# Performance work log

Measured on AMD Instinct MI355X. Metric: run time of the kernel, lower is better.

## Reference

```python
import jax, jax.numpy as jnp
import numpy as np

B, N, PL = 8, 961, 50          # batch, sequence_len=(64-4)//2+1 squared, patch_len=3*4^2+2
HID = 200                       # int(4.0 * patch_len)
D, H, HD = 768, 12, 64          # embed_dim, num_heads, head_dim
MP = 1536                       # int(2.0 * embed_dim)


def setup_inputs() -> dict:
    key = jax.random.key(0)
    ks = jax.random.split(key, 16)
    w = lambda k, i, o: jax.random.normal(k, (i, o), jnp.float32) / np.float32(np.sqrt(i))
    b = lambda k, o: jax.random.normal(k, (o,), jnp.float32) * np.float32(0.01)
    return {
        "x": jax.random.normal(ks[0], (B, N, PL), jnp.float32),
        "W1": w(ks[1], PL, HID),   "b1": b(ks[2], HID),
        "W2": w(ks[3], HID, HID),  "b2": b(ks[4], HID),
        "W3": w(ks[5], HID, HID),  "b3": b(ks[6], HID),
        "W4": w(ks[7], HID, D),    "b4": b(ks[8], D),
        "Wruv": w(ks[9], D, 3 * D), "bruv": b(ks[10], 3 * D),
        "Wp1": w(ks[11], N * HD, MP), "bp1": b(ks[12], MP),
        "Wp2": w(ks[13], MP, 1),      "bp2": b(ks[14], 1),
    }


def reference(x, W1, b1, W2, b2, W3, b3, W4, b4, Wruv, bruv, Wp1, bp1, Wp2, bp2):
    Bs, Ns, _ = x.shape
    # pointwise MLP (note: original has NO activations, just stacked Linears)
    h = x.reshape(Bs * Ns, -1)
    h = (((h @ W1 + b1) @ W2 + b2) @ W3 + b3) @ W4 + b4           # (B*N, D)
    # fused r,u,v projection -> (3, H, B, N, HD)
    ruv = (h @ Wruv + bruv).reshape(Bs, Ns, 3, H, HD).transpose(2, 3, 0, 1, 4)
    r, u, v = ruv[0], ruv[1], ruv[2]                               # each (H, B, N, HD)
    attn = jax.nn.softmax(jnp.einsum('hbnd,hbmd->hbnm', r, u), axis=-1)
    o = jnp.einsum('hbnm,hbmd->hbnd', attn, v).reshape(H, Bs, Ns * HD)
    # per-head projection: weights are SHARED across heads (list built via [m]*H)
    q = (jnp.einsum('hbm,mp->hbp', o, Wp1) + bp1) @ Wp2 + bp2      # (H, B, 1)
    return q[..., 0].T                                             # (B, 12)
```

## Files before the change

kernel.cpp:

```cpp
#include <hip/hip_runtime.h>
#include <hip/hip_bf16.h>

#define TPB 256

typedef __attribute__((ext_vector_type(8))) short bf16x8;
typedef __attribute__((ext_vector_type(4))) float f32x4;

static __device__ __forceinline__ unsigned short f2bf(float f) {
  union { float f; unsigned int u; } x; x.f = f;
  unsigned int r = x.u + 0x7FFF + ((x.u >> 16) & 1);
  return (unsigned short)(r >> 16);
}
static __device__ __forceinline__ float bf2f(unsigned short h) {
  union { unsigned int u; float f; } x; x.u = ((unsigned int)h) << 16;
  return x.f;
}

#define MFMA16(a, b, c) __builtin_amdgcn_mfma_f32_16x16x32_bf16(a, b, c, 0, 0, 0)

__global__ __launch_bounds__(TPB) void fold_wp_fused_k(
    const float* __restrict__ A, const float* __restrict__ lastrow,
    const float* __restrict__ W, const float* __restrict__ bias,
    float* __restrict__ C, int K, int Nc, int gemmBlocks,
    const float* __restrict__ Wp1, const float* __restrict__ Wp2,
    float* __restrict__ wfold, int wpStart, int wpCount,
    const float* __restrict__ bp1, const float* __restrict__ bp2,
    float* __restrict__ out)
{
  __shared__ float As[64][68];
  __shared__ float Ws[64][68];
  __shared__ float red[4];
  int bid = blockIdx.x, tid = threadIdx.x;

  if (bid >= gemmBlocks) {
    int u = bid - gemmBlocks;
    int wv = tid >> 6, lane = tid & 63;
    if (u >= wpCount) {
      float s = 0.f;
      for (int i = tid; i < 1536; i += TPB) s += bp1[i] * Wp2[i];
#pragma unroll
      for (int off = 32; off >= 1; off >>= 1) s += __shfl_xor(s, off, 64);
      if (lane == 0) red[wv] = s;
      __syncthreads();
      if (tid < 96) out[tid] = red[0] + red[1] + red[2] + red[3] + bp2[0];
      return;
    }
    float* w2 = &As[0][0];
    for (int i = tid; i < 1536; i += TPB) w2[i] = Wp2[i];
    __syncthreads();
    int m = (wpStart + u) * 4 + wv;
    const float* row = Wp1 + (size_t)m * 1536;
    float s = 0.f;
#pragma unroll
    for (int k = 0; k < 6; ++k) {
      float4 a  = *(const float4*)(row + k * 256 + lane * 4);
      float4 ww = *(const float4*)&w2[k * 256 + lane * 4];
      s += a.x * ww.x + a.y * ww.y + a.z * ww.z + a.w * ww.w;
    }
#pragma unroll
    for (int off = 32; off >= 1; off >>= 1) s += __shfl_xor(s, off, 64);
    if (lane == 0) wfold[m] = s;
    return;
  }

  int col0 = bid * 64;
  int ty = tid >> 4, tx = tid & 15;
  float acc[4][4] = {};
  for (int k0 = 0; k0 < K; k0 += 64) {
#pragma unroll
    for (int i = 0; i < 16; ++i) {
      int idx = tid + i * TPB;
      int r = idx >> 6, kk = idx & 63;
      int gk = k0 + kk;
      float v = 0.f;
      if (gk < K) {
        if (r < 50) v = A[(size_t)r * K + gk];
        else if (r == 50) v = lastrow[gk];
      }
      As[kk][r] = v;
    }
#pragma unroll
    for (int i = 0; i < 16; ++i) {
      int idx = tid + i * TPB;
      int kk = idx >> 6, cc = idx & 63;
      int gk = k0 + kk, gc = col0 + cc;
      float v = 0.f;
      if (gk < K && gc < Nc) v = W[(size_t)gk * Nc + gc];
      Ws[kk][cc] = v;
    }
    __syncthreads();
#pragma unroll 8
    for (int kk = 0; kk < 64; ++kk) {
      float4 a4 = *(const float4*)&As[kk][ty * 4];
      float4 b4 = *(const float4*)&Ws[kk][tx * 4];
      float av[4] = {a4.x, a4.y, a4.z, a4.w};
      float bv[4] = {b4.x, b4.y, b4.z, b4.w};
#pragma unroll
      for (int i = 0; i < 4; ++i)
#pragma unroll
        for (int j = 0; j < 4; ++j)
          acc[i][j] = fmaf(av[i], bv[j], acc[i][j]);
    }
    __syncthreads();
  }
#pragma unroll
  for (int i = 0; i < 4; ++i) {
    int gr = ty * 4 + i;
    if (gr >= 51) continue;
#pragma unroll
    for (int j = 0; j < 4; ++j) {
      int gc = col0 + tx * 4 + j;
      if (gc >= Nc) continue;
      float v = acc[i][j];
      if (gr == 50) v += bias[gc];
      C[(size_t)gr * Nc + gc] = v;
    }
  }
}

__global__ __launch_bounds__(TPB) void fold4_fused_k(
    const float* __restrict__ aug3,
    const float* __restrict__ Wruv,
    const float* __restrict__ bruv,
    unsigned short* __restrict__ WfTh, unsigned short* __restrict__ WfTl,
    float* __restrict__ bfv,
    const float* __restrict__ x,
    unsigned short* __restrict__ xh, unsigned short* __restrict__ xl,
    unsigned short* __restrict__ xT,
    const float* __restrict__ Wp1, const float* __restrict__ Wp2,
    float* __restrict__ wfold, int wpStart, int wpCount)
{
  __shared__ float As[64][68];
  __shared__ float Ws[64][68];
  int bid = blockIdx.x, tid = threadIdx.x;

  if (bid >= 157) {
    int u = bid - 157;
    if (u >= wpCount) return;
    int wv = tid >> 6, lane = tid & 63;
    float* w2 = &As[0][0];
    for (int i = tid; i < 1536; i += TPB) w2[i] = Wp2[i];
    __syncthreads();
    int m = (wpStart + u) * 4 + wv;
    const float* row = Wp1 + (size_t)m * 1536;
    float s = 0.f;
#pragma unroll
    for (int k = 0; k < 6; ++k) {
      float4 a  = *(const float4*)(row + k * 256 + lane * 4);
      float4 ww = *(const float4*)&w2[k * 256 + lane * 4];
      s += a.x * ww.x + a.y * ww.y + a.z * ww.z + a.w * ww.w;
    }
#pragma unroll
    for (int off = 32; off >= 1; off >>= 1) s += __shfl_xor(s, off, 64);
    if (lane == 0) wfold[m] = s;
    return;
  }

  if (bid >= 36) {
    int row0 = (bid - 36) * 64;
#pragma unroll
    for (int i = 0; i < 16; ++i) {
      int idx = tid + i * TPB;
      int row = row0 + (idx >> 6), cc = idx & 63;
      if (row >= 7688) continue;
      float v = 0.f;
      if (cc < 50) v = x[(size_t)row * 50 + cc];
      else if (cc == 50) v = 1.0f;
      unsigned short hi = f2bf(v);
      xh[(size_t)row * 64 + cc] = hi;
      xl[(size_t)row * 64 + cc] = f2bf(v - bf2f(hi));
      int bb = row / 961;
      int nl = row - bb * 961;
      xT[((size_t)bb * 64 + cc) * 968 + nl] = hi;
    }
    return;
  }

  const int K = 768, Nc = 2304;
  const float* lastrow = aug3 + (size_t)50 * 768;
  int col0 = bid * 64;
  int ty = tid >> 4, tx = tid & 15;
  float acc[4][4] = {};
  for (int k0 = 0; k0 < K; k0 += 64) {
#pragma unroll
    for (int i = 0; i < 16; ++i) {
      int idx = tid + i * TPB;
      int r = idx >> 6, kk = idx & 63;
      int gk = k0 + kk;
      float v = 0.f;
      if (r < 50) v = aug3[(size_t)r * K + gk];
      else if (r == 50) v = lastrow[gk];
      As[kk][r] = v;
    }
#pragma unroll
    for (int i = 0; i < 16; ++i) {
      int idx = tid + i * TPB;
      int kk = idx >> 6, cc = idx & 63;
      Ws[kk][cc] = Wruv[(size_t)(k0 + kk) * Nc + col0 + cc];
    }
    __syncthreads();
#pragma unroll 8
    for (int kk = 0; kk < 64; ++kk) {
      float4 a4 = *(const float4*)&As[kk][ty * 4];
      float4 b4 = *(const float4*)&Ws[kk][tx * 4];
      float av[4] = {a4.x, a4.y, a4.z, a4.w};
      float bv[4] = {b4.x, b4.y, b4.z, b4.w};
#pragma unroll
      for (int i = 0; i < 4; ++i)
#pragma unroll
        for (int j = 0; j < 4; ++j)
          acc[i][j] = fmaf(av[i], bv[j], acc[i][j]);
    }
    __syncthreads();
  }
#pragma unroll
  for (int i = 0; i < 4; ++i) {
    int gr = ty * 4 + i;
    if (gr >= 51) continue;
#pragma unroll
    for (int j = 0; j < 4; ++j) {
      int gc = col0 + tx * 4 + j;
      float v = acc[i][j];
      if (gr == 50) {
        bfv[gc] = v + bruv[gc];
      } else {
        unsigned short hi = f2bf(v);
        size_t el = (size_t)gc * 64 + gr;
        WfTh[el] = hi;
        WfTl[el] = f2bf(v - bf2f(hi));
      }
    }
  }
}

__global__ __launch_bounds__(TPB) void prep_k(
    const unsigned short* __restrict__ WfTh,
    const unsigned short* __restrict__ WfTl,
    const float* __restrict__ bfv,
    const float* __restrict__ wfold,
    unsigned short* __restrict__ Mth,
    unsigned short* __restrict__ Mtl,
    float* __restrict__ wvf)
{
  __shared__ float Al[64][64];
  __shared__ float Bl[64][64];
  int bid = blockIdx.x, tid = threadIdx.x;

  if (bid < 12) {
    int h = bid;
    for (int idx = tid; idx < 4096; idx += TPB) {
      int d = idx >> 6, i = idx & 63;
      int colr = h * 64 + d, colu = 768 + h * 64 + d;
      float wr = 0.f, wu = 0.f;
      if (i < 50) {
        wr = bf2f(WfTh[(size_t)colr * 64 + i]) + bf2f(WfTl[(size_t)colr * 64 + i]);
        wu = bf2f(WfTh[(size_t)colu * 64 + i]) + bf2f(WfTl[(size_t)colu * 64 + i]);
      } else if (i == 50) {
        wr = bfv[colr];
        wu = bfv[colu];
      }
      Al[d][i] = wr;
      Bl[d][i] = wu;
    }
    __syncthreads();
    for (int idx = tid; idx < 4096; idx += TPB) {
      int j = idx >> 6, i = idx & 63;
      float m = 0.f;
#pragma unroll 8
      for (int d = 0; d < 64; ++d) m += Al[d][i] * Bl[d][j];
      unsigned short hi = f2bf(m);
      size_t el = ((size_t)h * 64 + j) * 64 + i;
      Mth[el] = hi;
      Mtl[el] = f2bf(m - bf2f(hi));
    }
    return;
  }

  int u = bid - 12;
  int h = u >> 4, nb = u & 15;
  for (int idx = tid; idx < 4096; idx += TPB) {
    int d = idx >> 6, f = idx & 63;
    int colv = 1536 + h * 64 + d;
    float wv = 0.f;
    if (f < 50)
      wv = bf2f(WfTh[(size_t)colv * 64 + f]) + bf2f(WfTl[(size_t)colv * 64 + f]);
    else if (f == 50)
      wv = bfv[colv];
    Al[d][f] = wv;
    int nl = idx >> 6, dd = idx & 63;
    int n = nb * 64 + nl;
    Bl[nl][dd] = (n <= 960) ? wfold[(size_t)n * 64 + dd] : 0.f;
  }
  __syncthreads();
  for (int idx = tid; idx < 4096; idx += TPB) {
    int nl = idx >> 6, f = idx & 63;
    int n = nb * 64 + nl;
    if (n > 960) continue;
    float s = 0.f;
#pragma unroll 8
    for (int d = 0; d < 64; ++d) s += Bl[nl][d] * Al[d][f];
    wvf[((size_t)h * 961 + n) * 64 + f] = s;
  }
}

__global__ __launch_bounds__(512) void attn_x_k(
    const unsigned short* __restrict__ xh,
    const unsigned short* __restrict__ xl,
    const unsigned short* __restrict__ xT,
    const unsigned short* __restrict__ Mth,
    const unsigned short* __restrict__ Mtl,
    const float* __restrict__ wvf,
    float* __restrict__ out)
{
  __shared__ unsigned short sh[24576];
  int bid = blockIdx.x;
  int tid = threadIdx.x;

  int qb = bid & 7, hb = bid >> 3;
  int h = hb >> 3, b = hb & 7;
  int n0 = qb * 128;
  int w = tid >> 6, lane = tid & 63;
  int g = lane >> 4, c = lane & 15;
  int xb = b * 961;
  unsigned short* Kbuf[2] = {sh, sh + 4096};
  unsigned short* Vbuf[2] = {sh + 8192, sh + 12288};
  unsigned short* pw = sh + 16384 + w * 1024;

  int srow = tid >> 3, ss = tid & 7;
  int sel = srow * 64 + 8 * (ss ^ (srow & 7));
  const unsigned short* ksrc = xh + (size_t)xb * 64 + ss * 8;
  const unsigned short* vsrc = xT + ((size_t)b * 64 + srow) * 968 + ss * 8;
  int4 kv0 = *(const int4*)(ksrc + (size_t)srow * 64);
  int4 vv0 = *(const int4*)(vsrc);

  int qrow = n0 + w * 16 + c;
  if (qrow > 960) qrow = 960;
  size_t rowb = (size_t)(xb + qrow) * 64;
  bf16x8 axh0 = *(const bf16x8*)&xh[rowb + g * 8];
  bf16x8 axh1 = *(const bf16x8*)&xh[rowb + 32 + g * 8];
  bf16x8 axl0 = *(const bf16x8*)&xl[rowb + g * 8];
  bf16x8 axl1 = *(const bf16x8*)&xl[rowb + 32 + g * 8];

  f32x4 zero4 = {0.f, 0.f, 0.f, 0.f};
  f32x4 zacc[4] = {zero4, zero4, zero4, zero4};
#pragma unroll
  for (int ct = 0; ct < 4; ++ct) {
    int j = c * 4 + ct;
    size_t mb = ((size_t)h * 64 + j) * 64;
    bf16x8 bh0 = *(const bf16x8*)&Mth[mb + g * 8];
    bf16x8 bh1 = *(const bf16x8*)&Mth[mb + 32 + g * 8];
    bf16x8 bl0 = *(const bf16x8*)&Mtl[mb + g * 8];
    bf16x8 bl1 = *(const bf16x8*)&Mtl[mb + 32 + g * 8];
    zacc[ct] = MFMA16(axh0, bh0, zacc[ct]);
    zacc[ct] = MFMA16(axh1, bh1, zacc[ct]);
    zacc[ct] = MFMA16(axl0, bh0, zacc[ct]);
    zacc[ct] = MFMA16(axl1, bh1, zacc[ct]);
    zacc[ct] = MFMA16(axh0, bl0, zacc[ct]);
    zacc[ct] = MFMA16(axh1, bl1, zacc[ct]);
  }
#pragma unroll
  for (int r = 0; r < 4; ++r) {
    unsigned short pb[4];
#pragma unroll
    for (int ct = 0; ct < 4; ++ct) pb[ct] = f2bf(zacc[ct][r]);
    int q = g * 4 + r;
    int e0 = (c * 4) ^ ((q & 7) * 8);
    *(unsigned int*)&pw[q * 64 + e0] =
        (unsigned int)pb[0] | ((unsigned int)pb[1] << 16);
    *(unsigned int*)&pw[q * 64 + e0 + 2] =
        (unsigned int)pb[2] | ((unsigned int)pb[3] << 16);
  }
  bf16x8 zf0 = *(const bf16x8*)&pw[c * 64 + ((g * 8) ^ ((c & 7) * 8))];
  bf16x8 zf1 = *(const bf16x8*)&pw[c * 64 + ((32 + g * 8) ^ ((c & 7) * 8))];

  bf16x8 ones;
#pragma unroll
  for (int i = 0; i < 8; ++i) ones[i] = (short)0x3F80;

  *(int4*)&Kbuf[0][sel] = kv0;
  *(int4*)&Vbuf[0][sel] = vv0;
  __syncthreads();

  f32x4 pxacc[4] = {zero4, zero4, zero4, zero4};
  f32x4 rowacc = zero4;

  unsigned short* Kc = Kbuf[0];
  unsigned short* Vc = Vbuf[0];
  unsigned short* Kn = Kbuf[1];
  unsigned short* Vn = Vbuf[1];

  for (int kt = 0; kt < 16; ++kt) {
    int4 pk, pv;
    bool pre = (kt < 15);
    if (pre) {
      int keyg = (kt + 1) * 64 + srow;
      int kcl = keyg > 960 ? 960 : keyg;
      pk = *(const int4*)(ksrc + (size_t)kcl * 64);
      pv = *(const int4*)(vsrc + (kt + 1) * 64);
    }

    f32x4 sa[4] = {zero4, zero4, zero4, zero4};
    __builtin_amdgcn_s_setprio(1);
#pragma unroll
    for (int ct = 0; ct < 4; ++ct) {
      int key = c * 4 + ct;
      int sw = (key & 7) * 8;
      bf16x8 k0 = *(const bf16x8*)&Kc[key * 64 + ((g * 8) ^ sw)];
      bf16x8 k1 = *(const bf16x8*)&Kc[key * 64 + ((32 + g * 8) ^ sw)];
      sa[ct] = MFMA16(zf0, k0, sa[ct]);
      sa[ct] = MFMA16(zf1, k1, sa[ct]);
    }
    __builtin_amdgcn_s_setprio(0);

    if (kt < 15) {
#pragma unroll
      for (int r = 0; r < 4; ++r) {
        unsigned short pb[4];
#pragma unroll
        for (int ct = 0; ct < 4; ++ct)
          pb[ct] = f2bf(__expf(sa[ct][r]));
        int q = g * 4 + r;
        int e0 = (c * 4) ^ ((q & 7) * 8);
        *(unsigned int*)&pw[q * 64 + e0] =
            (unsigned int)pb[0] | ((unsigned int)pb[1] << 16);
        *(unsigned int*)&pw[q * 64 + e0 + 2] =
            (unsigned int)pb[2] | ((unsigned int)pb[3] << 16);
      }
    } else {
#pragma unroll
      for (int r = 0; r < 4; ++r) {
        unsigned short pb[4];
#pragma unroll
        for (int ct = 0; ct < 4; ++ct) {
          int keyg = kt * 64 + c * 4 + ct;
          pb[ct] = (keyg <= 960) ? f2bf(__expf(sa[ct][r])) : (unsigned short)0;
        }
        int q = g * 4 + r;
        int e0 = (c * 4) ^ ((q & 7) * 8);
        *(unsigned int*)&pw[q * 64 + e0] =
            (unsigned int)pb[0] | ((unsigned int)pb[1] << 16);
        *(unsigned int*)&pw[q * 64 + e0 + 2] =
            (unsigned int)pb[2] | ((unsigned int)pb[3] << 16);
      }
    }

    if (pre) {
      *(int4*)&Kn[sel] = pk;
      *(int4*)&Vn[sel] = pv;
    }

    __builtin_amdgcn_s_setprio(1);
#pragma unroll
    for (int kk = 0; kk < 2; ++kk) {
      bf16x8 pa = *(const bf16x8*)&pw[c * 64 + ((kk * 32 + g * 8) ^ ((c & 7) * 8))];
      rowacc = MFMA16(pa, ones, rowacc);
#pragma unroll
      for (int dt = 0; dt < 4; ++dt) {
        int d = dt * 16 + c;
        bf16x8 vf = *(const bf16x8*)&Vc[d * 64 + ((kk * 32 + g * 8) ^ ((d & 7) * 8))];
        pxacc[dt] = MFMA16(pa, vf, pxacc[dt]);
      }
    }
    __builtin_amdgcn_s_setprio(0);

    __syncthreads();
    unsigned short* t;
    t = Kc; Kc = Kn; Kn = t;
    t = Vc; Vc = Vn; Vn = t;
  }

  int nbase = n0 + w * 16 + g * 4;
  float part = 0.f;
#pragma unroll
  for (int r = 0; r < 4; ++r) {
    int n = nbase + r;
    if (n > 960) continue;
    float inv = 1.f / rowacc[r];
    const float* wv = wvf + ((size_t)h * 961 + n) * 64;
#pragma unroll
    for (int dt = 0; dt < 4; ++dt)
      part += pxacc[dt][r] * inv * wv[dt * 16 + c];
  }
#pragma unroll
  for (int off = 32; off >= 1; off >>= 1) part += __shfl_xor(part, off, 64);
  float* red = (float*)sh;
  if (lane == 0) red[w] = part;
  __syncthreads();
  if (tid == 0) {
    float tot = red[0] + red[1] + red[2] + red[3] +
                red[4] + red[5] + red[6] + red[7];
    atomicAdd(&out[b * 12 + h], tot);
  }
}

extern "C" void kernel_launch(void* const* d_in, const int* in_sizes, int n_in,
                              void* d_out, int out_size, void* d_ws, size_t ws_size,
                              hipStream_t stream)
{
  const float* x    = (const float*)d_in[0];
  const float* W1   = (const float*)d_in[1];
  const float* b1   = (const float*)d_in[2];
  const float* W2   = (const float*)d_in[3];
  const float* b2   = (const float*)d_in[4];
  const float* W3   = (const float*)d_in[5];
  const float* b3   = (const float*)d_in[6];
  const float* W4   = (const float*)d_in[7];
  const float* b4   = (const float*)d_in[8];
  const float* Wruv = (const float*)d_in[9];
  const float* bruv = (const float*)d_in[10];
  const float* Wp1  = (const float*)d_in[11];
  const float* bp1  = (const float*)d_in[12];
  const float* Wp2  = (const float*)d_in[13];
  const float* bp2  = (const float*)d_in[14];
  float* out = (float*)d_out;

  char* base = (char*)d_ws;
  size_t off = 0;
  auto alloc = [&](size_t bytes) -> void* {
    void* p = base + off;
    off = (off + bytes + 255) & ~(size_t)255;
    return p;
  };
  float* aug1  = (float*)alloc(51 * 200 * 4);
  float* aug2  = (float*)alloc(51 * 200 * 4);
  float* aug3  = (float*)alloc(51 * 768 * 4);
  unsigned short* WfTh = (unsigned short*)alloc((size_t)2304 * 64 * 2);
  unsigned short* WfTl = (unsigned short*)alloc((size_t)2304 * 64 * 2);
  unsigned short* xh   = (unsigned short*)alloc((size_t)(7688 + 64) * 64 * 2);
  unsigned short* xl   = (unsigned short*)alloc((size_t)(7688 + 64) * 64 * 2);
  unsigned short* xT   = (unsigned short*)alloc((size_t)8 * 64 * 968 * 2 + 1024);
  unsigned short* Mth  = (unsigned short*)alloc((size_t)12 * 64 * 64 * 2);
  unsigned short* Mtl  = (unsigned short*)alloc((size_t)12 * 64 * 64 * 2);
  float* wvf   = (float*)alloc((size_t)12 * 961 * 64 * 4);
  float* bfv   = (float*)alloc(2304 * 4);
  float* wfold = (float*)alloc(61504 * 4);
  if (off > ws_size) return;

  dim3 tb(TPB);

  fold_wp_fused_k<<<dim3(4 + 3844 + 1), tb, 0, stream>>>(
      W1, b1, W2, b2, aug1, 200, 200, 4,
      Wp1, Wp2, wfold, 0, 3844, bp1, bp2, out);
  fold_wp_fused_k<<<dim3(4 + 3844), tb, 0, stream>>>(
      aug1, aug1 + 50 * 200, W3, b3, aug2, 200, 200, 4,
      Wp1, Wp2, wfold, 3844, 3844, bp1, bp2, out);
  fold_wp_fused_k<<<dim3(12 + 3844), tb, 0, stream>>>(
      aug2, aug2 + 50 * 200, W4, b4, aug3, 200, 768, 12,
      Wp1, Wp2, wfold, 7688, 3844, bp1, bp2, out);

  fold4_fused_k<<<dim3(157 + 3844), tb, 0, stream>>>(
      aug3, Wruv, bruv, WfTh, WfTl, bfv, x, xh, xl, xT,
      Wp1, Wp2, wfold, 11532, 3844);

  prep_k<<<dim3(204), tb, 0, stream>>>(WfTh, WfTl, bfv, wfold, Mth, Mtl, wvf);

  attn_x_k<<<dim3(768), dim3(512), 0, stream>>>(xh, xl, xT, Mth, Mtl, wvf, out);
}
```

Baseline: 317.6 us.

## Overlap Wp1 folding with attention and defer value projection to final kernel

Shrinks the Wp1·Wp2 folding spread across the earlier fold kernels and moves the remaining rows into extra blocks of the attention kernel, so that weight-streaming work overlaps with attention compute. The attention epilogue now writes the normalized P·V outputs to a large Y buffer instead of dotting them with a precomputed per-head wvf. A new final kernel contracts Y with wfold and the V projection weights to produce the outputs. The precomputed wvf stage is dropped, at the cost of an extra round trip of about 24MB through global memory and one more launch.

```diff
diff --git a/kernel.cpp b/kernel.cpp
--- a/kernel.cpp
+++ b/kernel.cpp
@@ -233,88 +233,78 @@
   }
 }
 
-__global__ __launch_bounds__(TPB) void prep_k(
+__global__ __launch_bounds__(TPB) void prepM_k(
     const unsigned short* __restrict__ WfTh,
     const unsigned short* __restrict__ WfTl,
     const float* __restrict__ bfv,
-    const float* __restrict__ wfold,
     unsigned short* __restrict__ Mth,
-    unsigned short* __restrict__ Mtl,
-    float* __restrict__ wvf)
+    unsigned short* __restrict__ Mtl)
 {
   __shared__ float Al[64][64];
   __shared__ float Bl[64][64];
-  int bid = blockIdx.x, tid = threadIdx.x;
-
-  if (bid < 12) {
-    int h = bid;
-    for (int idx = tid; idx < 4096; idx += TPB) {
-      int d = idx >> 6, i = idx & 63;
-      int colr = h * 64 + d, colu = 768 + h * 64 + d;
-      float wr = 0.f, wu = 0.f;
-      if (i < 50) {
-        wr = bf2f(WfTh[(size_t)colr * 64 + i]) + bf2f(WfTl[(size_t)colr * 64 + i]);
-        wu = bf2f(WfTh[(size_t)colu * 64 + i]) + bf2f(WfTl[(size_t)colu * 64 + i]);
-      } else if (i == 50) {
-        wr = bfv[colr];
-        wu = bfv[colu];
-      }
-      Al[d][i] = wr;
-      Bl[d][i] = wu;
-    }
-    __syncthreads();
-    for (int idx = tid; idx < 4096; idx += TPB) {
-      int j = idx >> 6, i = idx & 63;
-      float m = 0.f;
-#pragma unroll 8
-      for (int d = 0; d < 64; ++d) m += Al[d][i] * Bl[d][j];
-      unsigned short hi = f2bf(m);
-      size_t el = ((size_t)h * 64 + j) * 64 + i;
-      Mth[el] = hi;
-      Mtl[el] = f2bf(m - bf2f(hi));
-    }
-    return;
-  }
-
-  int u = bid - 12;
-  int h = u >> 4, nb = u & 15;
+  int h = blockIdx.x, tid = threadIdx.x;
+
   for (int idx = tid; idx < 4096; idx += TPB) {
-    int d = idx >> 6, f = idx & 63;
-    int colv = 1536 + h * 64 + d;
-    float wv = 0.f;
-    if (f < 50)
-      wv = bf2f(WfTh[(size_t)colv * 64 + f]) + bf2f(WfTl[(size_t)colv * 64 + f]);
-    else if (f == 50)
-      wv = bfv[colv];
-    Al[d][f] = wv;
-    int nl = idx >> 6, dd = idx & 63;
-    int n = nb * 64 + nl;
-    Bl[nl][dd] = (n <= 960) ? wfold[(size_t)n * 64 + dd] : 0.f;
+    int d = idx >> 6, i = idx & 63;
+    int colr = h * 64 + d, colu = 768 + h * 64 + d;
+    float wr = 0.f, wu = 0.f;
+    if (i < 50) {
+      wr = bf2f(WfTh[(size_t)colr * 64 + i]) + bf2f(WfTl[(size_t)colr * 64 + i]);
+      wu = bf2f(WfTh[(size_t)colu * 64 + i]) + bf2f(WfTl[(size_t)colu * 64 + i]);
+    } else if (i == 50) {
+      wr = bfv[colr];
+      wu = bfv[colu];
+    }
+    Al[d][i] = wr;
+    Bl[d][i] = wu;
   }
   __syncthreads();
   for (int idx = tid; idx < 4096; idx += TPB) {
-    int nl = idx >> 6, f = idx & 63;
-    int n = nb * 64 + nl;
-    if (n > 960) continue;
-    float s = 0.f;
+    int j = idx >> 6, i = idx & 63;
+    float m = 0.f;
 #pragma unroll 8
-    for (int d = 0; d < 64; ++d) s += Bl[nl][d] * Al[d][f];
-    wvf[((size_t)h * 961 + n) * 64 + f] = s;
-  }
-}
-
-__global__ __launch_bounds__(512) void attn_x_k(
+    for (int d = 0; d < 64; ++d) m += Al[d][i] * Bl[d][j];
+    unsigned short hi = f2bf(m);
+    size_t el = ((size_t)h * 64 + j) * 64 + i;
+    Mth[el] = hi;
+    Mtl[el] = f2bf(m - bf2f(hi));
+  }
+}
+
+__global__ __launch_bounds__(512) void attn_wp_y_k(
     const unsigned short* __restrict__ xh,
     const unsigned short* __restrict__ xl,
     const unsigned short* __restrict__ xT,
     const unsigned short* __restrict__ Mth,
     const unsigned short* __restrict__ Mtl,
-    const float* __restrict__ wvf,
-    float* __restrict__ out)
+    float* __restrict__ Y,
+    const float* __restrict__ Wp1, const float* __restrict__ Wp2,
+    float* __restrict__ wfold)
 {
   __shared__ unsigned short sh[24576];
   int bid = blockIdx.x;
   int tid = threadIdx.x;
+
+  if (bid >= 768) {
+    int u = bid - 768;
+    int wv = tid >> 6, lane = tid & 63;
+    float* w2 = (float*)sh;
+    for (int i = tid; i < 1536; i += 512) w2[i] = Wp2[i];
+    __syncthreads();
+    int m = 25600 + u * 8 + wv;
+    const float* row = Wp1 + (size_t)m * 1536;
+    float s = 0.f;
+#pragma unroll
+    for (int k = 0; k < 6; ++k) {
+      float4 a  = *(const float4*)(row + k * 256 + lane * 4);
+      float4 ww = *(const float4*)&w2[k * 256 + lane * 4];
+      s += a.x * ww.x + a.y * ww.y + a.z * ww.z + a.w * ww.w;
+    }
+#pragma unroll
+    for (int off = 32; off >= 1; off >>= 1) s += __shfl_xor(s, off, 64);
+    if (lane == 0) wfold[m] = s;
+    return;
+  }
 
   int qb = bid & 7, hb = bid >> 3;
   int h = hb >> 3, b = hb & 7;
@@ -470,27 +460,85 @@
   }
 
   int nbase = n0 + w * 16 + g * 4;
-  float part = 0.f;
+  float* yb = Y + (size_t)hb * 961 * 64;
 #pragma unroll
   for (int r = 0; r < 4; ++r) {
     int n = nbase + r;
     if (n > 960) continue;
     float inv = 1.f / rowacc[r];
-    const float* wv = wvf + ((size_t)h * 961 + n) * 64;
 #pragma unroll
     for (int dt = 0; dt < 4; ++dt)
-      part += pxacc[dt][r] * inv * wv[dt * 16 + c];
-  }
-#pragma unroll
-  for (int off = 32; off >= 1; off >>= 1) part += __shfl_xor(part, off, 64);
-  float* red = (float*)sh;
-  if (lane == 0) red[w] = part;
+      yb[(size_t)n * 64 + dt * 16 + c] = pxacc[dt][r] * inv;
+  }
+}
+
+__global__ __launch_bounds__(TPB) void final_k(
+    const float* __restrict__ Y,
+    const float* __restrict__ wfold,
+    const unsigned short* __restrict__ WfTh,
+    const unsigned short* __restrict__ WfTl,
+    const float* __restrict__ bfv,
+    float* __restrict__ out)
+{
+  __shared__ float yl[64][64];
+  __shared__ float wl[64][64];
+  __shared__ float red[4];
+  int hb = blockIdx.x;
+  int h = hb >> 3, b = hb & 7;
+  int tid = threadIdx.x;
+  int f = tid >> 2, d16 = (tid & 3) * 16;
+  float T[16] = {};
+  const float* ybase = Y + (size_t)hb * 961 * 64;
+
+  for (int t0 = 0; t0 < 961; t0 += 64) {
+    int rows = 961 - t0 < 64 ? 961 - t0 : 64;
+    for (int idx = tid; idx < 4096; idx += TPB) {
+      int nl = idx >> 6, dd = idx & 63;
+      float yv = 0.f, wv = 0.f;
+      if (nl < rows) {
+        yv = ybase[(size_t)(t0 + nl) * 64 + dd];
+        wv = wfold[(size_t)(t0 + nl) * 64 + dd];
+      }
+      yl[nl][dd] = yv;
+      wl[nl][dd] = wv;
+    }
+    __syncthreads();
+    for (int nl = 0; nl < 64; ++nl) {
+      float yv = yl[nl][f];
+      float4 w0 = *(const float4*)&wl[nl][d16];
+      float4 w1 = *(const float4*)&wl[nl][d16 + 4];
+      float4 w2 = *(const float4*)&wl[nl][d16 + 8];
+      float4 w3 = *(const float4*)&wl[nl][d16 + 12];
+      T[0] = fmaf(yv, w0.x, T[0]);   T[1] = fmaf(yv, w0.y, T[1]);
+      T[2] = fmaf(yv, w0.z, T[2]);   T[3] = fmaf(yv, w0.w, T[3]);
+      T[4] = fmaf(yv, w1.x, T[4]);   T[5] = fmaf(yv, w1.y, T[5]);
+      T[6] = fmaf(yv, w1.z, T[6]);   T[7] = fmaf(yv, w1.w, T[7]);
+      T[8] = fmaf(yv, w2.x, T[8]);   T[9] = fmaf(yv, w2.y, T[9]);
+      T[10] = fmaf(yv, w2.z, T[10]); T[11] = fmaf(yv, w2.w, T[11]);
+      T[12] = fmaf(yv, w3.x, T[12]); T[13] = fmaf(yv, w3.y, T[13]);
+      T[14] = fmaf(yv, w3.z, T[14]); T[15] = fmaf(yv, w3.w, T[15]);
+    }
+    __syncthreads();
+  }
+
+  float s = 0.f;
+  if (f <= 50) {
+#pragma unroll
+    for (int j = 0; j < 16; ++j) {
+      int d = d16 + j;
+      int colv = 1536 + h * 64 + d;
+      float wv;
+      if (f == 50) wv = bfv[colv];
+      else wv = bf2f(WfTh[(size_t)colv * 64 + f]) + bf2f(WfTl[(size_t)colv * 64 + f]);
+      s = fmaf(T[j], wv, s);
+    }
+  }
+  int lane = tid & 63, wvv = tid >> 6;
+#pragma unroll
+  for (int off = 32; off >= 1; off >>= 1) s += __shfl_xor(s, off, 64);
+  if (lane == 0) red[wvv] = s;
   __syncthreads();
-  if (tid == 0) {
-    float tot = red[0] + red[1] + red[2] + red[3] +
-                red[4] + red[5] + red[6] + red[7];
-    atomicAdd(&out[b * 12 + h], tot);
-  }
+  if (tid == 0) out[b * 12 + h] += red[0] + red[1] + red[2] + red[3];
 }
 
 extern "C" void kernel_launch(void* const* d_in, const int* in_sizes, int n_in,
@@ -531,28 +579,31 @@
   unsigned short* xT   = (unsigned short*)alloc((size_t)8 * 64 * 968 * 2 + 1024);
   unsigned short* Mth  = (unsigned short*)alloc((size_t)12 * 64 * 64 * 2);
   unsigned short* Mtl  = (unsigned short*)alloc((size_t)12 * 64 * 64 * 2);
-  float* wvf   = (float*)alloc((size_t)12 * 961 * 64 * 4);
+  float* Yb    = (float*)alloc((size_t)96 * 961 * 64 * 4);
   float* bfv   = (float*)alloc(2304 * 4);
   float* wfold = (float*)alloc(61504 * 4);
   if (off > ws_size) return;
 
   dim3 tb(TPB);
 
-  fold_wp_fused_k<<<dim3(4 + 3844 + 1), tb, 0, stream>>>(
+  fold_wp_fused_k<<<dim3(4 + 1600 + 1), tb, 0, stream>>>(
       W1, b1, W2, b2, aug1, 200, 200, 4,
-      Wp1, Wp2, wfold, 0, 3844, bp1, bp2, out);
-  fold_wp_fused_k<<<dim3(4 + 3844), tb, 0, stream>>>(
+      Wp1, Wp2, wfold, 0, 1600, bp1, bp2, out);
+  fold_wp_fused_k<<<dim3(4 + 1600), tb, 0, stream>>>(
       aug1, aug1 + 50 * 200, W3, b3, aug2, 200, 200, 4,
-      Wp1, Wp2, wfold, 3844, 3844, bp1, bp2, out);
-  fold_wp_fused_k<<<dim3(12 + 3844), tb, 0, stream>>>(
+      Wp1, Wp2, wfold, 1600, 1600, bp1, bp2, out);
+  fold_wp_fused_k<<<dim3(12 + 1600), tb, 0, stream>>>(
       aug2, aug2 + 50 * 200, W4, b4, aug3, 200, 768, 12,
-      Wp1, Wp2, wfold, 7688, 3844, bp1, bp2, out);
-
-  fold4_fused_k<<<dim3(157 + 3844), tb, 0, stream>>>(
+      Wp1, Wp2, wfold, 3200, 1600, bp1, bp2, out);
+
+  fold4_fused_k<<<dim3(157 + 1600), tb, 0, stream>>>(
       aug3, Wruv, bruv, WfTh, WfTl, bfv, x, xh, xl, xT,
-      Wp1, Wp2, wfold, 11532, 3844);
-
-  prep_k<<<dim3(204), tb, 0, stream>>>(WfTh, WfTl, bfv, wfold, Mth, Mtl, wvf);
-
-  attn_x_k<<<dim3(768), dim3(512), 0, stream>>>(xh, xl, xT, Mth, Mtl, wvf, out);
-}
+      Wp1, Wp2, wfold, 4800, 1600);
+
+  prepM_k<<<dim3(12), tb, 0, stream>>>(WfTh, WfTl, bfv, Mth, Mtl);
+
+  attn_wp_y_k<<<dim3(768 + 4488), dim3(512), 0, stream>>>(
+      xh, xl, xT, Mth, Mtl, Yb, Wp1, Wp2, wfold);
+
+  final_k<<<dim3(96), tb, 0, stream>>>(Yb, wfold, WfTh, WfTl, bfv, out);
+}
```

After: 453.0 us. 42.6% more time.
